# Optimization experiments

Hardware: AMD Instinct MI355X
Metric: run time of the kernel (lower is better)

## Reference

```python
import jax, jax.numpy as jnp
import numpy as np

H = 51  # hidden size fixed by the module

def _gru_cell(x, h, w_ih, w_hh, b_ih, b_hh):
    # PyTorch GRUCell math. w_ih: [3H, in], w_hh: [3H, H]
    gi = x @ w_ih.T + b_ih          # [B, 3H]
    gh = h @ w_hh.T + b_hh          # [B, 3H]
    i_r, i_z, i_n = jnp.split(gi, 3, axis=-1)
    h_r, h_z, h_n = jnp.split(gh, 3, axis=-1)
    r = jax.nn.sigmoid(i_r + h_r)
    z = jax.nn.sigmoid(i_z + h_z)
    n = jnp.tanh(i_n + r * h_n)
    return (1.0 - z) * n + z * h


def setup_inputs() -> dict:
    key = jax.random.key(0)
    ks = jax.random.split(key, 11)
    B, T = 2048, 1000
    s = 1.0 / np.sqrt(H)  # torch default init scale
    u = lambda k, shape: jax.random.uniform(k, shape, jnp.float32, -s, s)
    return {
        "x": jax.random.normal(ks[0], (B, T), jnp.float32),
        "w_ih1": u(ks[1], (3 * H, 1)),
        "w_hh1": u(ks[2], (3 * H, H)),
        "b_ih1": u(ks[3], (3 * H,)),
        "b_hh1": u(ks[4], (3 * H,)),
        "w_ih2": u(ks[5], (3 * H, H)),
        "w_hh2": u(ks[6], (3 * H, H)),
        "b_ih2": u(ks[7], (3 * H,)),
        "b_hh2": u(ks[8], (3 * H,)),
        "w_lin": u(ks[9], (1, H)),
        "b_lin": u(ks[10], (1,)),
        "future_steps": 1000,
    }


def reference(x, w_ih1, w_hh1, b_ih1, b_hh1, w_ih2, w_hh2, b_ih2, b_hh2,
              w_lin, b_lin, future_steps):
    B = x.shape[0]
    h1 = jnp.zeros((B, H), x.dtype)
    h2 = jnp.zeros((B, H), x.dtype)

    def step(carry, xt):  # xt: [B, 1]
        h1, h2 = carry
        h1 = _gru_cell(xt, h1, w_ih1, w_hh1, b_ih1, b_hh1)
        h2 = _gru_cell(h1, h2, w_ih2, w_hh2, b_ih2, b_hh2)
        out = h2 @ w_lin.T + b_lin  # [B, 1]
        return (h1, h2), out

    xs = jnp.swapaxes(x, 0, 1)[:, :, None]  # [T, B, 1]
    (h1, h2), outs1 = jax.lax.scan(step, (h1, h2), xs)

    def fstep(carry, _):
        h1, h2, out = carry
        h1 = _gru_cell(out, h1, w_ih1, w_hh1, b_ih1, b_hh1)
        h2 = _gru_cell(h1, h2, w_ih2, w_hh2, b_ih2, b_hh2)
        out = h2 @ w_lin.T + b_lin
        return (h1, h2, out), out

    last = outs1[-1]
    (_, _, _), outs2 = jax.lax.scan(fstep, (h1, h2, last), None,
                                    length=future_steps)

    outs = jnp.concatenate([outs1, outs2], axis=0)  # [T+F, B, 1]
    return jnp.swapaxes(outs[:, :, 0], 0, 1)        # [B, T+F]
```

## Files before the change

kernel.cpp:

```cpp
#include <hip/hip_runtime.h>
#include <hip/hip_bf16.h>

#define HH 51
#define TPB 512
#define BPB 8
#define US 36

typedef _Float16 half8 __attribute__((ext_vector_type(8)));
typedef float f4 __attribute__((ext_vector_type(4)));

#define LBAR() asm volatile("s_waitcnt lgkmcnt(0)\ns_barrier" ::: "memory")

__device__ __forceinline__ float bf2f(unsigned short u) {
    return __uint_as_float(((unsigned)u) << 16);
}
__device__ __forceinline__ float loadf(const void* p, size_t i, bool bf) {
    return bf ? bf2f(((const unsigned short*)p)[i]) : ((const float*)p)[i];
}
__device__ __forceinline__ void storef(void* p, size_t i, float v, bool bf) {
    if (bf) ((__hip_bfloat16*)p)[i] = __float2bfloat16(v);
    else    ((float*)p)[i] = v;
}
__device__ __forceinline__ float sigm(float v) {
    return __builtin_amdgcn_rcpf(1.0f + __expf(-v));
}
__device__ __forceinline__ float tanh_fast(float v) {
    return fmaf(2.0f, __builtin_amdgcn_rcpf(1.0f + __expf(-2.0f * v)), -1.0f);
}
__device__ __forceinline__ f4 MF(half8 a, half8 b, f4 c) {
    return __builtin_amdgcn_mfma_f32_16x16x32_f16(a, b, c, 0, 0, 0);
}
__device__ __forceinline__ float wave_sum(float x) {
    float s = x, t;
    t = __builtin_bit_cast(float, __builtin_amdgcn_update_dpp(0, __builtin_bit_cast(int, s), 0x111, 0xf, 0xf, true)); s += t;
    t = __builtin_bit_cast(float, __builtin_amdgcn_update_dpp(0, __builtin_bit_cast(int, s), 0x112, 0xf, 0xf, true)); s += t;
    t = __builtin_bit_cast(float, __builtin_amdgcn_update_dpp(0, __builtin_bit_cast(int, s), 0x114, 0xf, 0xf, true)); s += t;
    t = __builtin_bit_cast(float, __builtin_amdgcn_update_dpp(0, __builtin_bit_cast(int, s), 0x118, 0xf, 0xf, true)); s += t;
    t = __builtin_bit_cast(float, __builtin_amdgcn_update_dpp(0, __builtin_bit_cast(int, s), 0x142, 0xa, 0xf, true)); s += t;
    t = __builtin_bit_cast(float, __builtin_amdgcn_update_dpp(0, __builtin_bit_cast(int, s), 0x143, 0xc, 0xf, true)); s += t;
    return __builtin_bit_cast(float, __builtin_amdgcn_readlane(__builtin_bit_cast(int, s), 63));
}
__device__ __forceinline__ float rdlane(float v, int idx) {
    return __builtin_bit_cast(float, __builtin_amdgcn_readlane(__builtin_bit_cast(int, v), idx));
}

__global__ __launch_bounds__(TPB, 1) void gru_kernel(
    const void* __restrict__ xg,
    const void* __restrict__ wih1, const void* __restrict__ whh1,
    const void* __restrict__ bih1, const void* __restrict__ bhh1,
    const void* __restrict__ wih2, const void* __restrict__ whh2,
    const void* __restrict__ bih2, const void* __restrict__ bhh2,
    const void* __restrict__ wlin, const void* __restrict__ blin_p,
    void* __restrict__ dout, int T, int TF)
{
    __shared__ __align__(16) _Float16 stg[208 * 64];
    __shared__ __align__(16) float gbuf1[52 * US];
    __shared__ __align__(16) float gbuf2[52 * US];
    __shared__ __align__(16) _Float16 h1T[2][16 * 72];
    __shared__ __align__(16) _Float16 h2T[2][16 * 72];
    __shared__ float obufL[BPB * 64];
    __shared__ float hfin[2][BPB * 52];

    const int tid = threadIdx.x, w = tid >> 6, lane = tid & 63;
    const int n16 = lane & 15, q = lane >> 4;
    const bool li = lane < HH;
    const int il = li ? lane : HH - 1;
    const int bg0 = blockIdx.x * BPB;
    const int myb = bg0 + w;

    bool isbf;
    {
        const unsigned short* u = (const unsigned short*)whh1;
        int ok = 1;
#pragma unroll
        for (int k = 0; k < 16; ++k) {
            unsigned e = (u[2 * k] >> 7) & 0xFF;
            ok &= (e >= 100 && e <= 125) ? 1 : 0;
        }
        isbf = (ok != 0);
    }

    float wr1 = 0, wz1 = 0, wn1 = 0, wl = 0;
    if (li) {
        wr1 = loadf(wih1, il, isbf);          wz1 = loadf(wih1, HH + il, isbf);
        wn1 = loadf(wih1, 2 * HH + il, isbf); wl = loadf(wlin, il, isbf);
    }
    const float blv = loadf(blin_p, 0, isbf);

    const int nm1 = (w < 5) ? 2 : 1;
    int m2a, m2b, nm2;
    if (w < 2)      { m2a = w + 3; m2b = w + 11; nm2 = 2; }
    else if (w < 5) { m2a = w + 3; m2b = 0;      nm2 = 1; }
    else            { m2a = w - 5; m2b = w + 3;  nm2 = 2; }
    const int m1t[2] = { w, w + 8 };
    const int m2t[2] = { m2a, m2b };
    const int laneoff = q * US + 4 * n16;
    const bool stlane = (n16 < 8);
    const bool outw = (w == 1);

    half8 WfM1[2][2], WfM2[2][4];

#pragma unroll 1
    for (int ps = 0; ps < 3; ++ps) {
        for (int e = tid; e < 208 * 64; e += TPB) {
            int r = e >> 6, k = e & 63;
            int u = r >> 2, g = r & 3;
            float v = 0.0f;
            if (ps == 0) {
                if (u < HH) {
                    if (g < 2) {
                        int gr = g * HH + u;
                        if (k < HH) v = loadf(whh1, (size_t)gr * HH + k, isbf);
                        else if (k == 52) v = loadf(bhh1, gr, isbf) + loadf(bih1, gr, isbf);
                        else if (k == 53) v = loadf(wih1, gr, isbf);
                    } else if (g == 2) {
                        int gr = 2 * HH + u;
                        if (k < HH) v = loadf(whh1, (size_t)gr * HH + k, isbf);
                        else if (k == 52) v = loadf(bhh1, gr, isbf);
                    } else {
                        int gr = 2 * HH + u;
                        if (k == 52) v = loadf(bih1, gr, isbf);
                        else if (k == 53) v = loadf(wih1, gr, isbf);
                    }
                }
            } else if (ps == 1) {
                if (u < HH) {
                    if (g < 2) {
                        int gr = g * HH + u;
                        if (k < HH) v = loadf(whh2, (size_t)gr * HH + k, isbf);
                        else if (k == 52) v = loadf(bhh2, gr, isbf) + loadf(bih2, gr, isbf);
                    } else if (g == 2) {
                        int gr = 2 * HH + u;
                        if (k < HH) v = loadf(whh2, (size_t)gr * HH + k, isbf);
                        else if (k == 52) v = loadf(bhh2, gr, isbf);
                    } else {
                        if (k == 52) v = loadf(bih2, 2 * HH + u, isbf);
                    }
                } else if (r == 204) {
                    if (k < HH) v = loadf(wlin, k, isbf);
                    else if (k == 52) v = blv;
                }
            } else {
                if (u < HH) {
                    if (g < 2) {
                        if (k < HH) v = loadf(wih2, (size_t)(g * HH + u) * HH + k, isbf);
                    } else if (g == 3) {
                        if (k < HH) v = loadf(wih2, (size_t)(2 * HH + u) * HH + k, isbf);
                    }
                }
            }
            stg[e] = (_Float16)v;
        }
        __syncthreads();
        if (ps == 0) {
#pragma unroll
            for (int i = 0; i < 2; ++i) if (i < nm1) {
                int tl = m1t[i];
                WfM1[i][0] = *(const half8*)(stg + (size_t)(16 * tl + n16) * 64 + q * 8);
                WfM1[i][1] = *(const half8*)(stg + (size_t)(16 * tl + n16) * 64 + 32 + q * 8);
            }
        } else if (ps == 1) {
#pragma unroll
            for (int i = 0; i < 2; ++i) if (i < nm2) {
                int tl = m2t[i];
                WfM2[i][0] = *(const half8*)(stg + (size_t)(16 * tl + n16) * 64 + q * 8);
                WfM2[i][1] = *(const half8*)(stg + (size_t)(16 * tl + n16) * 64 + 32 + q * 8);
            }
        } else {
#pragma unroll
            for (int i = 0; i < 2; ++i) if (i < nm2) {
                int tl = m2t[i];
                WfM2[i][2] = *(const half8*)(stg + (size_t)(16 * tl + n16) * 64 + q * 8);
                WfM2[i][3] = *(const half8*)(stg + (size_t)(16 * tl + n16) * 64 + 32 + q * 8);
            }
        }
        __syncthreads();
    }

    for (int e = tid; e < 16 * 72; e += TPB) {
        h1T[0][e] = (_Float16)0; h1T[1][e] = (_Float16)0;
        h2T[0][e] = (_Float16)0; h2T[1][e] = (_Float16)0;
    }
    float xreg = 0.0f, xnext = 0.0f;
    if (lane < T) xreg = loadf(xg, (size_t)myb * T + lane, isbf);
    __syncthreads();
    if (tid < 16) {
        h1T[0][tid * 72 + 52] = (_Float16)1.0f; h1T[1][tid * 72 + 52] = (_Float16)1.0f;
        h2T[0][tid * 72 + 52] = (_Float16)1.0f; h2T[1][tid * 72 + 52] = (_Float16)1.0f;
    }
    if (lane == 0) h1T[1][w * 72 + 53] = (_Float16)rdlane(xreg, 0);
    __syncthreads();

    float h1s[2] = {0.f, 0.f}, h2s[2] = {0.f, 0.f};

    const int ro0 = n16 * 72 + q * 8, ro1 = ro0 + 32;
    int wo1[2], wo2[2];
    bool stw1[2], stw2[2];
#pragma unroll
    for (int i = 0; i < 2; ++i) {
        int u1 = 4 * m1t[i] + q, u2 = 4 * m2t[i] + q;
        wo1[i] = n16 * 72 + u1; stw1[i] = (n16 < 8) && (u1 < HH);
        wo2[i] = n16 * 72 + u2; stw2[i] = (n16 < 8) && (u2 < HH);
    }
    const bool obl = outw && (q == 3) && (n16 < 8);
    const int s1o[2] = { m1t[0] * 4 * US + laneoff, m1t[1] * 4 * US + laneoff };
    const int s2o[2] = { m2t[0] * 4 * US + laneoff, m2t[1] * 4 * US + laneoff };

#define ENC_BODY(T_, H1R, H2R, H1W, H2W, DOM2, DOOUT)                          \
    {                                                                          \
        half8 H10 = *(const half8*)((H1R) + ro0);                              \
        half8 H11 = *(const half8*)((H1R) + ro1);                              \
        half8 H20 = *(const half8*)((H2R) + ro0);                              \
        half8 H21 = *(const half8*)((H2R) + ro1);                              \
        {                                                                      \
            int ni = ((T_) + 1) & 63;                                          \
            float xsrc = (ni == 0) ? xnext : xreg;                             \
            float xnv = ((T_) == T - 1) ? 0.0f : rdlane(xsrc, ni);             \
            if (lane == 0) (H1W)[w * 72 + 53] = (_Float16)xnv;                 \
        }                                                                      \
        _Pragma("unroll")                                                      \
        for (int i = 0; i < 2; ++i) if (i < nm1) {                             \
            f4 a = {0.f, 0.f, 0.f, 0.f};                                       \
            a = MF(WfM1[i][0], H10, a); a = MF(WfM1[i][1], H11, a);            \
            float r = sigm(a[0]), z = sigm(a[1]);                              \
            float n = tanh_fast(fmaf(r, a[2], a[3]));                          \
            float h = fmaf(z, h1s[i] - n, n); h1s[i] = h;                      \
            if (stw1[i]) (H1W)[wo1[i]] = (_Float16)h;                          \
        }                                                                      \
        if (DOM2) {                                                            \
            _Pragma("unroll")                                                  \
            for (int i = 0; i < 2; ++i) if (i < nm2) {                         \
                f4 a = {0.f, 0.f, 0.f, 0.f}, b = {0.f, 0.f, 0.f, 0.f};         \
                a = MF(WfM2[i][0], H20, a); a = MF(WfM2[i][1], H21, a);        \
                b = MF(WfM2[i][2], H10, b); b = MF(WfM2[i][3], H11, b);        \
                a = a + b;                                                     \
                if ((DOOUT) && i == 1 && obl)                                  \
                    obufL[n16 * 64 + (((T_) - 2) & 63)] = a[0];                \
                float r2 = sigm(a[0]), z2 = sigm(a[1]);                        \
                float n2 = tanh_fast(fmaf(r2, a[2], a[3]));                    \
                float h = fmaf(z2, h2s[i] - n2, n2); h2s[i] = h;               \
                if (stw2[i]) (H2W)[wo2[i]] = (_Float16)h;                      \
            }                                                                  \
        }                                                                      \
    }

    ENC_BODY(0, h1T[1], h2T[1], h1T[0], h2T[0], false, false);
    if (64 < T) {
        int src = 64 + lane;
        xnext = (src < T) ? loadf(xg, (size_t)myb * T + src, isbf) : 0.0f;
    }
    LBAR();
    ENC_BODY(1, h1T[0], h2T[0], h1T[1], h2T[1], true, false);
    LBAR();
    for (int t = 2; t < T; t += 2) {
        ENC_BODY(t, h1T[1], h2T[1], h1T[0], h2T[0], true, true);
        if (w >= 6 && (t & 31) == 2 && t >= 34) {
            int fb = t - 34;
#pragma unroll
            for (int k2 = 0; k2 < 2; ++k2) {
                int et = ((w - 6) << 7) + (k2 << 6) + lane;
                int b2 = et >> 5, tt = et & 31;
                storef(dout, (size_t)(bg0 + b2) * TF + fb + tt, obufL[b2 * 64 + ((fb + tt) & 63)], isbf);
            }
        }
        if ((t & 63) == 0) {
            int base = t + 64;
            if (base < T) {
                int src = base + lane;
                xnext = (src < T) ? loadf(xg, (size_t)myb * T + src, isbf) : 0.0f;
            }
        }
        LBAR();
        ENC_BODY(t + 1, h1T[0], h2T[0], h1T[1], h2T[1], true, true);
        if (((t + 1) & 63) == 63) xreg = xnext;
        LBAR();
    }

    const int fbi = (T + 1) & 1;
    {
        const _Float16* h1r = h1T[fbi];
        const _Float16* h2r = h2T[fbi];
        half8 H10 = *(const half8*)(h1r + ro0);
        half8 H11 = *(const half8*)(h1r + ro1);
        half8 H20 = *(const half8*)(h2r + ro0);
        half8 H21 = *(const half8*)(h2r + ro1);
#pragma unroll
        for (int i = 0; i < 2; ++i) if (i < nm1) {
            f4 a = {0.f, 0.f, 0.f, 0.f};
            a = MF(WfM1[i][0], H10, a); a = MF(WfM1[i][1], H11, a);
            if (stlane) *(f4*)(gbuf1 + s1o[i]) = a;
            int u = 4 * m1t[i] + q;
            if (n16 < 8 && u < HH) hfin[0][n16 * 52 + u] = h1s[i];
        }
#pragma unroll
        for (int i = 0; i < 2; ++i) if (i < nm2) {
            f4 a = {0.f, 0.f, 0.f, 0.f}, b = {0.f, 0.f, 0.f, 0.f};
            a = MF(WfM2[i][0], H20, a); a = MF(WfM2[i][1], H21, a);
            b = MF(WfM2[i][2], H10, b); b = MF(WfM2[i][3], H11, b);
            a = a + b;
            if (stlane) *(f4*)(gbuf2 + s2o[i]) = a;
            int u = 4 * m2t[i] + q;
            if (n16 < 8 && u < HH) hfin[1][n16 * 52 + u] = h2s[i];
        }
    }
    __syncthreads();

    float h1p = hfin[0][w * 52 + il];
    float h2p = hfin[1][w * 52 + il];
    const float* gl1 = gbuf1 + il * US + 4 * w;
    const float* gl2 = gbuf2 + il * US + 4 * w;
    const int or2 = 51 * US;
    _Float16* fh1 = h1T[fbi];
    _Float16* fh2 = h2T[fbi];

    if (lane == 0) obufL[w * 64 + ((T - 2) & 63)] = gbuf2[or2 + 4 * w];

#define FB_STEP(T_, DOFLUSH)                                                   \
    {                                                                          \
        f4 G1 = *(const f4*)gl1;                                               \
        f4 G2 = *(const f4*)gl2;                                               \
        float r2 = sigm(G2[0]), z2 = sigm(G2[1]);                              \
        float n2 = tanh_fast(fmaf(r2, G2[2], G2[3]));                          \
        float hh2 = fmaf(z2, h2p - n2, n2); h2p = hh2;                         \
        float p = 0.0f;                                                        \
        if (li) { fh2[w * 72 + il] = (_Float16)hh2; p = hh2 * wl; }            \
        float outv = wave_sum(p) + blv;                                        \
        if (lane == 0) obufL[w * 64 + (((T_) - 1) & 63)] = outv;               \
        float r = sigm(fmaf(outv, wr1, G1[0]));                                \
        float z = sigm(fmaf(outv, wz1, G1[1]));                                \
        float n = tanh_fast(fmaf(r, G1[2], fmaf(outv, wn1, G1[3])));           \
        float hh1 = fmaf(z, h1p - n, n); h1p = hh1;                            \
        if (li) fh1[w * 72 + il] = (_Float16)hh1;                              \
        LBAR();                                                                \
        {                                                                      \
            half8 H10 = *(const half8*)(fh1 + ro0);                            \
            half8 H11 = *(const half8*)(fh1 + ro1);                            \
            half8 H20 = *(const half8*)(fh2 + ro0);                            \
            half8 H21 = *(const half8*)(fh2 + ro1);                            \
            _Pragma("unroll")                                                  \
            for (int i = 0; i < 2; ++i) if (i < nm1) {                         \
                f4 a = {0.f, 0.f, 0.f, 0.f};                                   \
                a = MF(WfM1[i][0], H10, a); a = MF(WfM1[i][1], H11, a);        \
                if (stlane) *(f4*)(gbuf1 + s1o[i]) = a;                        \
            }                                                                  \
            _Pragma("unroll")                                                  \
            for (int i = 0; i < 2; ++i) if (i < nm2) {                         \
                f4 a = {0.f, 0.f, 0.f, 0.f}, b = {0.f, 0.f, 0.f, 0.f};         \
                a = MF(WfM2[i][0], H20, a); a = MF(WfM2[i][1], H21, a);        \
                b = MF(WfM2[i][2], H10, b); b = MF(WfM2[i][3], H11, b);        \
                a = a + b;                                                     \
                if (stlane) *(f4*)(gbuf2 + s2o[i]) = a;                        \
            }                                                                  \
        }                                                                      \
        if ((DOFLUSH) && w >= 6 && ((T_) & 31) == 0) {                         \
            int fb = (T_) - 32;                                                \
            _Pragma("unroll")                                                  \
            for (int k2 = 0; k2 < 2; ++k2) {                                   \
                int et = ((w - 6) << 7) + (k2 << 6) + lane;                    \
                int b2 = et >> 5, tt = et & 31;                                \
                storef(dout, (size_t)(bg0 + b2) * TF + fb + tt,                \
                       obufL[b2 * 64 + ((fb + tt) & 63)], isbf);               \
            }                                                                  \
        }                                                                      \
        LBAR();                                                                \
    }

    for (int t = T; t < TF; t += 2) {
        FB_STEP(t, true);
        FB_STEP(t + 1, false);
    }

    {
        f4 G2 = *(const f4*)gl2;
        float p = 0.0f;
        float r2 = sigm(G2[0]), z2 = sigm(G2[1]);
        float n2 = tanh_fast(fmaf(r2, G2[2], G2[3]));
        float h = fmaf(z2, h2p - n2, n2);
        if (li) p = h * wl;
        float osum = wave_sum(p) + blv;
        if (lane == 0) obufL[w * 64 + ((TF - 1) & 63)] = osum;
    }
    __syncthreads();
    {
        int base = (TF - 1) & ~31, rem = TF - base;
        if (tid < BPB * 32) {
            int b2 = tid >> 5, tt = tid & 31;
            if (tt < rem)
                storef(dout, (size_t)(bg0 + b2) * TF + base + tt, obufL[b2 * 64 + ((base + tt) & 63)], isbf);
        }
    }
}

extern "C" void kernel_launch(void* const* d_in, const int* in_sizes, int n_in,
                              void* d_out, int out_size, void* d_ws, size_t ws_size,
                              hipStream_t stream) {
    const int B = 2048;
    const int T = in_sizes[0] / B;
    const int TF = out_size / B;
    gru_kernel<<<dim3(B / BPB), dim3(TPB), 0, stream>>>(
        d_in[0], d_in[1], d_in[2], d_in[3], d_in[4], d_in[5],
        d_in[6], d_in[7], d_in[8], d_in[9], d_in[10],
        d_out, T, TF);
}
```

Before: 1.463 ms.

## Double block to 16 waves so each wave owns one MFMA tile per layer

Raises threads per block from 512 to 1024. Each of the 16 waves now holds at most one layer-1 tile and one layer-2 tile instead of up to two of each, which shortens the serial per-step MFMA and gate chain on every wave. The batch-specific decoder work stays on the first 8 waves, and the output flush is remapped to waves 0-3. In exchange the per-step barriers now synchronise twice as many waves, register pressure and occupancy limits change, and half the waves sit idle during the decoder's elementwise phase.

```diff
diff --git a/kernel.cpp b/kernel.cpp
--- a/kernel.cpp
+++ b/kernel.cpp
@@ -2,7 +2,7 @@
 #include <hip/hip_bf16.h>
 
 #define HH 51
-#define TPB 512
+#define TPB 1024
 #define BPB 8
 #define US 36
 
@@ -66,7 +66,8 @@
     const bool li = lane < HH;
     const int il = li ? lane : HH - 1;
     const int bg0 = blockIdx.x * BPB;
-    const int myb = bg0 + w;
+    const bool bw = (w < 8);
+    const int myb = bg0 + (w & 7);
 
     bool isbf;
     {
@@ -87,18 +88,15 @@
     }
     const float blv = loadf(blin_p, 0, isbf);
 
-    const int nm1 = (w < 5) ? 2 : 1;
-    int m2a, m2b, nm2;
-    if (w < 2)      { m2a = w + 3; m2b = w + 11; nm2 = 2; }
-    else if (w < 5) { m2a = w + 3; m2b = 0;      nm2 = 1; }
-    else            { m2a = w - 5; m2b = w + 3;  nm2 = 2; }
-    const int m1t[2] = { w, w + 8 };
-    const int m2t[2] = { m2a, m2b };
+    const bool hasM1 = (w < 13);
+    const bool hasM2 = (w >= 3);
+    const int m1tl = w;
+    const int m2tl = 15 - w;
     const int laneoff = q * US + 4 * n16;
     const bool stlane = (n16 < 8);
-    const bool outw = (w == 1);
-
-    half8 WfM1[2][2], WfM2[2][4];
+    const bool obl = (w == 3) && (q == 3) && (n16 < 8);
+
+    half8 WfM1[2], WfM2[4];
 
 #pragma unroll 1
     for (int ps = 0; ps < 3; ++ps) {
@@ -152,27 +150,15 @@
             stg[e] = (_Float16)v;
         }
         __syncthreads();
-        if (ps == 0) {
-#pragma unroll
-            for (int i = 0; i < 2; ++i) if (i < nm1) {
-                int tl = m1t[i];
-                WfM1[i][0] = *(const half8*)(stg + (size_t)(16 * tl + n16) * 64 + q * 8);
-                WfM1[i][1] = *(const half8*)(stg + (size_t)(16 * tl + n16) * 64 + 32 + q * 8);
-            }
-        } else if (ps == 1) {
-#pragma unroll
-            for (int i = 0; i < 2; ++i) if (i < nm2) {
-                int tl = m2t[i];
-                WfM2[i][0] = *(const half8*)(stg + (size_t)(16 * tl + n16) * 64 + q * 8);
-                WfM2[i][1] = *(const half8*)(stg + (size_t)(16 * tl + n16) * 64 + 32 + q * 8);
-            }
-        } else {
-#pragma unroll
-            for (int i = 0; i < 2; ++i) if (i < nm2) {
-                int tl = m2t[i];
-                WfM2[i][2] = *(const half8*)(stg + (size_t)(16 * tl + n16) * 64 + q * 8);
-                WfM2[i][3] = *(const half8*)(stg + (size_t)(16 * tl + n16) * 64 + 32 + q * 8);
-            }
+        if (ps == 0 && hasM1) {
+            WfM1[0] = *(const half8*)(stg + (size_t)(16 * m1tl + n16) * 64 + q * 8);
+            WfM1[1] = *(const half8*)(stg + (size_t)(16 * m1tl + n16) * 64 + 32 + q * 8);
+        } else if (ps == 1 && hasM2) {
+            WfM2[0] = *(const half8*)(stg + (size_t)(16 * m2tl + n16) * 64 + q * 8);
+            WfM2[1] = *(const half8*)(stg + (size_t)(16 * m2tl + n16) * 64 + 32 + q * 8);
+        } else if (ps == 2 && hasM2) {
+            WfM2[2] = *(const half8*)(stg + (size_t)(16 * m2tl + n16) * 64 + q * 8);
+            WfM2[3] = *(const half8*)(stg + (size_t)(16 * m2tl + n16) * 64 + 32 + q * 8);
         }
         __syncthreads();
     }
@@ -182,70 +168,61 @@
         h2T[0][e] = (_Float16)0; h2T[1][e] = (_Float16)0;
     }
     float xreg = 0.0f, xnext = 0.0f;
-    if (lane < T) xreg = loadf(xg, (size_t)myb * T + lane, isbf);
+    if (bw && lane < T) xreg = loadf(xg, (size_t)myb * T + lane, isbf);
     __syncthreads();
     if (tid < 16) {
         h1T[0][tid * 72 + 52] = (_Float16)1.0f; h1T[1][tid * 72 + 52] = (_Float16)1.0f;
         h2T[0][tid * 72 + 52] = (_Float16)1.0f; h2T[1][tid * 72 + 52] = (_Float16)1.0f;
     }
-    if (lane == 0) h1T[1][w * 72 + 53] = (_Float16)rdlane(xreg, 0);
+    if (bw && lane == 0) h1T[1][w * 72 + 53] = (_Float16)rdlane(xreg, 0);
     __syncthreads();
 
-    float h1s[2] = {0.f, 0.f}, h2s[2] = {0.f, 0.f};
+    float h1sv = 0.f, h2sv = 0.f;
 
     const int ro0 = n16 * 72 + q * 8, ro1 = ro0 + 32;
-    int wo1[2], wo2[2];
-    bool stw1[2], stw2[2];
-#pragma unroll
-    for (int i = 0; i < 2; ++i) {
-        int u1 = 4 * m1t[i] + q, u2 = 4 * m2t[i] + q;
-        wo1[i] = n16 * 72 + u1; stw1[i] = (n16 < 8) && (u1 < HH);
-        wo2[i] = n16 * 72 + u2; stw2[i] = (n16 < 8) && (u2 < HH);
-    }
-    const bool obl = outw && (q == 3) && (n16 < 8);
-    const int s1o[2] = { m1t[0] * 4 * US + laneoff, m1t[1] * 4 * US + laneoff };
-    const int s2o[2] = { m2t[0] * 4 * US + laneoff, m2t[1] * 4 * US + laneoff };
+    const int u1 = 4 * m1tl + q, u2 = 4 * m2tl + q;
+    const int wo1 = n16 * 72 + u1, wo2 = n16 * 72 + u2;
+    const bool stw1 = hasM1 && (n16 < 8) && (u1 < HH);
+    const bool stw2 = hasM2 && (n16 < 8) && (u2 < HH);
+    const int s1o = m1tl * 4 * US + laneoff;
+    const int s2o = m2tl * 4 * US + laneoff;
 
 #define ENC_BODY(T_, H1R, H2R, H1W, H2W, DOM2, DOOUT)                          \
     {                                                                          \
         half8 H10 = *(const half8*)((H1R) + ro0);                              \
         half8 H11 = *(const half8*)((H1R) + ro1);                              \
-        half8 H20 = *(const half8*)((H2R) + ro0);                              \
-        half8 H21 = *(const half8*)((H2R) + ro1);                              \
         {                                                                      \
             int ni = ((T_) + 1) & 63;                                          \
             float xsrc = (ni == 0) ? xnext : xreg;                             \
             float xnv = ((T_) == T - 1) ? 0.0f : rdlane(xsrc, ni);             \
-            if (lane == 0) (H1W)[w * 72 + 53] = (_Float16)xnv;                 \
-        }                                                                      \
-        _Pragma("unroll")                                                      \
-        for (int i = 0; i < 2; ++i) if (i < nm1) {                             \
+            if (bw && lane == 0) (H1W)[w * 72 + 53] = (_Float16)xnv;           \
+        }                                                                      \
+        if (hasM1) {                                                           \
             f4 a = {0.f, 0.f, 0.f, 0.f};                                       \
-            a = MF(WfM1[i][0], H10, a); a = MF(WfM1[i][1], H11, a);            \
+            a = MF(WfM1[0], H10, a); a = MF(WfM1[1], H11, a);                  \
             float r = sigm(a[0]), z = sigm(a[1]);                              \
             float n = tanh_fast(fmaf(r, a[2], a[3]));                          \
-            float h = fmaf(z, h1s[i] - n, n); h1s[i] = h;                      \
-            if (stw1[i]) (H1W)[wo1[i]] = (_Float16)h;                          \
-        }                                                                      \
-        if (DOM2) {                                                            \
-            _Pragma("unroll")                                                  \
-            for (int i = 0; i < 2; ++i) if (i < nm2) {                         \
-                f4 a = {0.f, 0.f, 0.f, 0.f}, b = {0.f, 0.f, 0.f, 0.f};         \
-                a = MF(WfM2[i][0], H20, a); a = MF(WfM2[i][1], H21, a);        \
-                b = MF(WfM2[i][2], H10, b); b = MF(WfM2[i][3], H11, b);        \
-                a = a + b;                                                     \
-                if ((DOOUT) && i == 1 && obl)                                  \
-                    obufL[n16 * 64 + (((T_) - 2) & 63)] = a[0];                \
-                float r2 = sigm(a[0]), z2 = sigm(a[1]);                        \
-                float n2 = tanh_fast(fmaf(r2, a[2], a[3]));                    \
-                float h = fmaf(z2, h2s[i] - n2, n2); h2s[i] = h;               \
-                if (stw2[i]) (H2W)[wo2[i]] = (_Float16)h;                      \
-            }                                                                  \
+            float h = fmaf(z, h1sv - n, n); h1sv = h;                          \
+            if (stw1) (H1W)[wo1] = (_Float16)h;                                \
+        }                                                                      \
+        if ((DOM2) && hasM2) {                                                 \
+            half8 H20 = *(const half8*)((H2R) + ro0);                          \
+            half8 H21 = *(const half8*)((H2R) + ro1);                          \
+            f4 a = {0.f, 0.f, 0.f, 0.f}, b = {0.f, 0.f, 0.f, 0.f};             \
+            a = MF(WfM2[0], H20, a); a = MF(WfM2[1], H21, a);                  \
+            b = MF(WfM2[2], H10, b); b = MF(WfM2[3], H11, b);                  \
+            a = a + b;                                                         \
+            if ((DOOUT) && obl)                                                \
+                obufL[n16 * 64 + (((T_) - 2) & 63)] = a[0];                    \
+            float r2 = sigm(a[0]), z2 = sigm(a[1]);                            \
+            float n2 = tanh_fast(fmaf(r2, a[2], a[3]));                        \
+            float h = fmaf(z2, h2sv - n2, n2); h2sv = h;                       \
+            if (stw2) (H2W)[wo2] = (_Float16)h;                                \
         }                                                                      \
     }
 
     ENC_BODY(0, h1T[1], h2T[1], h1T[0], h2T[0], false, false);
-    if (64 < T) {
+    if (bw && 64 < T) {
         int src = 64 + lane;
         xnext = (src < T) ? loadf(xg, (size_t)myb * T + src, isbf) : 0.0f;
     }
@@ -254,16 +231,13 @@
     LBAR();
     for (int t = 2; t < T; t += 2) {
         ENC_BODY(t, h1T[1], h2T[1], h1T[0], h2T[0], true, true);
-        if (w >= 6 && (t & 31) == 2 && t >= 34) {
+        if (w < 4 && (t & 31) == 2 && t >= 34) {
             int fb = t - 34;
-#pragma unroll
-            for (int k2 = 0; k2 < 2; ++k2) {
-                int et = ((w - 6) << 7) + (k2 << 6) + lane;
-                int b2 = et >> 5, tt = et & 31;
-                storef(dout, (size_t)(bg0 + b2) * TF + fb + tt, obufL[b2 * 64 + ((fb + tt) & 63)], isbf);
-            }
-        }
-        if ((t & 63) == 0) {
+            int et = (w << 6) + lane;
+            int b2 = et >> 5, tt = et & 31;
+            storef(dout, (size_t)(bg0 + b2) * TF + fb + tt, obufL[b2 * 64 + ((fb + tt) & 63)], isbf);
+        }
+        if (bw && (t & 63) == 0) {
             int base = t + 64;
             if (base < T) {
                 int src = base + lane;
@@ -282,85 +256,78 @@
         const _Float16* h2r = h2T[fbi];
         half8 H10 = *(const half8*)(h1r + ro0);
         half8 H11 = *(const half8*)(h1r + ro1);
-        half8 H20 = *(const half8*)(h2r + ro0);
-        half8 H21 = *(const half8*)(h2r + ro1);
-#pragma unroll
-        for (int i = 0; i < 2; ++i) if (i < nm1) {
+        if (hasM1) {
             f4 a = {0.f, 0.f, 0.f, 0.f};
-            a = MF(WfM1[i][0], H10, a); a = MF(WfM1[i][1], H11, a);
-            if (stlane) *(f4*)(gbuf1 + s1o[i]) = a;
-            int u = 4 * m1t[i] + q;
-            if (n16 < 8 && u < HH) hfin[0][n16 * 52 + u] = h1s[i];
-        }
-#pragma unroll
-        for (int i = 0; i < 2; ++i) if (i < nm2) {
+            a = MF(WfM1[0], H10, a); a = MF(WfM1[1], H11, a);
+            if (stlane) *(f4*)(gbuf1 + s1o) = a;
+            if (n16 < 8 && u1 < HH) hfin[0][n16 * 52 + u1] = h1sv;
+        }
+        if (hasM2) {
+            half8 H20 = *(const half8*)(h2r + ro0);
+            half8 H21 = *(const half8*)(h2r + ro1);
             f4 a = {0.f, 0.f, 0.f, 0.f}, b = {0.f, 0.f, 0.f, 0.f};
-            a = MF(WfM2[i][0], H20, a); a = MF(WfM2[i][1], H21, a);
-            b = MF(WfM2[i][2], H10, b); b = MF(WfM2[i][3], H11, b);
+            a = MF(WfM2[0], H20, a); a = MF(WfM2[1], H21, a);
+            b = MF(WfM2[2], H10, b); b = MF(WfM2[3], H11, b);
             a = a + b;
-            if (stlane) *(f4*)(gbuf2 + s2o[i]) = a;
-            int u = 4 * m2t[i] + q;
-            if (n16 < 8 && u < HH) hfin[1][n16 * 52 + u] = h2s[i];
+            if (stlane) *(f4*)(gbuf2 + s2o) = a;
+            if (n16 < 8 && u2 < HH) hfin[1][n16 * 52 + u2] = h2sv;
         }
     }
     __syncthreads();
 
-    float h1p = hfin[0][w * 52 + il];
-    float h2p = hfin[1][w * 52 + il];
-    const float* gl1 = gbuf1 + il * US + 4 * w;
-    const float* gl2 = gbuf2 + il * US + 4 * w;
+    float h1p = bw ? hfin[0][w * 52 + il] : 0.0f;
+    float h2p = bw ? hfin[1][w * 52 + il] : 0.0f;
+    const float* gl1 = gbuf1 + il * US + 4 * (w & 7);
+    const float* gl2 = gbuf2 + il * US + 4 * (w & 7);
     const int or2 = 51 * US;
     _Float16* fh1 = h1T[fbi];
     _Float16* fh2 = h2T[fbi];
 
-    if (lane == 0) obufL[w * 64 + ((T - 2) & 63)] = gbuf2[or2 + 4 * w];
+    if (bw && lane == 0) obufL[w * 64 + ((T - 2) & 63)] = gbuf2[or2 + 4 * w];
 
 #define FB_STEP(T_, DOFLUSH)                                                   \
     {                                                                          \
-        f4 G1 = *(const f4*)gl1;                                               \
-        f4 G2 = *(const f4*)gl2;                                               \
-        float r2 = sigm(G2[0]), z2 = sigm(G2[1]);                              \
-        float n2 = tanh_fast(fmaf(r2, G2[2], G2[3]));                          \
-        float hh2 = fmaf(z2, h2p - n2, n2); h2p = hh2;                         \
-        float p = 0.0f;                                                        \
-        if (li) { fh2[w * 72 + il] = (_Float16)hh2; p = hh2 * wl; }            \
-        float outv = wave_sum(p) + blv;                                        \
-        if (lane == 0) obufL[w * 64 + (((T_) - 1) & 63)] = outv;               \
-        float r = sigm(fmaf(outv, wr1, G1[0]));                                \
-        float z = sigm(fmaf(outv, wz1, G1[1]));                                \
-        float n = tanh_fast(fmaf(r, G1[2], fmaf(outv, wn1, G1[3])));           \
-        float hh1 = fmaf(z, h1p - n, n); h1p = hh1;                            \
-        if (li) fh1[w * 72 + il] = (_Float16)hh1;                              \
+        if (bw) {                                                              \
+            f4 G1 = *(const f4*)gl1;                                           \
+            f4 G2 = *(const f4*)gl2;                                           \
+            float r2 = sigm(G2[0]), z2 = sigm(G2[1]);                          \
+            float n2 = tanh_fast(fmaf(r2, G2[2], G2[3]));                      \
+            float hh2 = fmaf(z2, h2p - n2, n2); h2p = hh2;                     \
+            float p = 0.0f;                                                    \
+            if (li) { fh2[w * 72 + il] = (_Float16)hh2; p = hh2 * wl; }        \
+            float outv = wave_sum(p) + blv;                                    \
+            if (lane == 0) obufL[w * 64 + (((T_) - 1) & 63)] = outv;           \
+            float r = sigm(fmaf(outv, wr1, G1[0]));                            \
+            float z = sigm(fmaf(outv, wz1, G1[1]));                            \
+            float n = tanh_fast(fmaf(r, G1[2], fmaf(outv, wn1, G1[3])));       \
+            float hh1 = fmaf(z, h1p - n, n); h1p = hh1;                        \
+            if (li) fh1[w * 72 + il] = (_Float16)hh1;                          \
+        }                                                                      \
         LBAR();                                                                \
         {                                                                      \
             half8 H10 = *(const half8*)(fh1 + ro0);                            \
             half8 H11 = *(const half8*)(fh1 + ro1);                            \
-            half8 H20 = *(const half8*)(fh2 + ro0);                            \
-            half8 H21 = *(const half8*)(fh2 + ro1);                            \
-            _Pragma("unroll")                                                  \
-            for (int i = 0; i < 2; ++i) if (i < nm1) {                         \
+            if (hasM1) {                                                       \
                 f4 a = {0.f, 0.f, 0.f, 0.f};                                   \
-                a = MF(WfM1[i][0], H10, a); a = MF(WfM1[i][1], H11, a);        \
-                if (stlane) *(f4*)(gbuf1 + s1o[i]) = a;                        \
+                a = MF(WfM1[0], H10, a); a = MF(WfM1[1], H11, a);              \
+                if (stlane) *(f4*)(gbuf1 + s1o) = a;                           \
             }                                                                  \
-            _Pragma("unroll")                                                  \
-            for (int i = 0; i < 2; ++i) if (i < nm2) {                         \
+            if (hasM2) {                                                       \
+                half8 H20 = *(const half8*)(fh2 + ro0);                        \
+                half8 H21 = *(const half8*)(fh2 + ro1);                        \
                 f4 a = {0.f, 0.f, 0.f, 0.f}, b = {0.f, 0.f, 0.f, 0.f};         \
-                a = MF(WfM2[i][0], H20, a); a = MF(WfM2[i][1], H21, a);        \
-                b = MF(WfM2[i][2], H10, b); b = MF(WfM2[i][3], H11, b);        \
+                a = MF(WfM2[0], H20, a); a = MF(WfM2[1], H21, a);              \
+                b = MF(WfM2[2], H10, b); b = MF(WfM2[3], H11, b);              \
                 a = a + b;                                                     \
-                if (stlane) *(f4*)(gbuf2 + s2o[i]) = a;                        \
+                if (stlane) *(f4*)(gbuf2 + s2o) = a;                           \
             }                                                                  \
         }                                                                      \
-        if ((DOFLUSH) && w >= 6 && ((T_) & 31) == 0) {                         \
+        if ((DOFLUSH) && w < 4 && ((T_) & 31) == 0) {                          \
             int fb = (T_) - 32;                                                \
-            _Pragma("unroll")                                                  \
-            for (int k2 = 0; k2 < 2; ++k2) {                                   \
-                int et = ((w - 6) << 7) + (k2 << 6) + lane;                    \
-                int b2 = et >> 5, tt = et & 31;                                \
-                storef(dout, (size_t)(bg0 + b2) * TF + fb + tt,                \
-                       obufL[b2 * 64 + ((fb + tt) & 63)], isbf);               \
-            }                                                                  \
+            int et = (w << 6) + lane;                                          \
+            int b2 = et >> 5, tt = et & 31;                                    \
+            storef(dout, (size_t)(bg0 + b2) * TF + fb + tt,                    \
+                   obufL[b2 * 64 + ((fb + tt) & 63)], isbf);                   \
         }                                                                      \
         LBAR();                                                                \
     }
@@ -370,7 +337,7 @@
         FB_STEP(t + 1, false);
     }
 
-    {
+    if (bw) {
         f4 G2 = *(const f4*)gl2;
         float p = 0.0f;
         float r2 = sigm(G2[0]), z2 = sigm(G2[1]);
```

Result: no change. 1.453 ms (-0.7%).
